# Optimization experiments

Measured on AMD Instinct MI355X. Metric: run time of the kernel, lower is better.

Reference implementation:

```python
import jax, jax.numpy as jnp
import numpy as np
import math

B, NQ, D = 2, 5000, 256
HEADS, LVLS, PTS, NREF = 8, 4, 8, 4  # PTS = all_sampling_points, NREF = ref points per query
DH = D // HEADS
SHAPES = [(100, 100), (50, 50), (25, 25), (13, 13)]
NV = sum(h * w for h, w in SHAPES)


def _grid_init_bias():
    # replicates DeformableSatAttention.init_weights sampling_offsets bias
    thetas = np.arange(HEADS, dtype=np.float32) * (2.0 * math.pi / HEADS)
    grid = np.stack([np.cos(thetas), np.sin(thetas)], -1)
    grid = grid / np.abs(grid).max(-1, keepdims=True)
    grid = np.tile(grid.reshape(HEADS, 1, 1, 2), (1, LVLS, PTS, 1))  # PTS == HEADS
    for i in range(PTS):
        grid[:, :, i, :] *= i + 1
    return jnp.asarray(grid.reshape(-1), dtype=jnp.float32)


def setup_inputs() -> dict:
    key = jax.random.key(0)
    ks = jax.random.split(key, 8)
    xb = math.sqrt(6.0 / (D + D))  # xavier uniform bound for value_proj
    return {
        "query": jax.random.normal(ks[0], (B, NQ, D), jnp.float32),
        "key": jax.random.normal(ks[1], (B, NV, D), jnp.float32),
        "value": jax.random.normal(ks[2], (B, NV, D), jnp.float32),
        "reference_points": jax.random.uniform(ks[3], (B, NQ, NREF, 2), jnp.float32),
        "spatial_shapes": jnp.asarray(SHAPES, jnp.int32),
        "level_start_index": jnp.asarray(np.cumsum([0] + [h * w for h, w in SHAPES])[:-1], jnp.int32),
        "W_value": jax.random.uniform(ks[4], (D, D), jnp.float32, -xb, xb),
        "b_value": jnp.zeros((D,), jnp.float32),
        "W_offset": 0.01 * jax.random.normal(ks[5], (D, HEADS * LVLS * PTS * 2), jnp.float32),
        "b_offset": _grid_init_bias(),
        "W_attn": 0.01 * jax.random.normal(ks[6], (D, HEADS * LVLS * PTS), jnp.float32),
        "b_attn": jnp.zeros((HEADS * LVLS * PTS,), jnp.float32),
    }


def _bilinear(vflat, H, W, loc):
    # vflat: [B, H*W, HEADS, DH]; loc: [B, NQ, HEADS, PTS, 2] in [0,1]
    # grid_sample-style align_corners=False, zero padding (as in MSDeformAttn CUDA)
    x = loc[..., 0] * W - 0.5
    y = loc[..., 1] * H - 0.5
    x0 = jnp.floor(x)
    y0 = jnp.floor(y)
    dx = x - x0
    dy = y - y0
    x0i = x0.astype(jnp.int32)
    y0i = y0.astype(jnp.int32)

    def gather(ix, iy):
        valid = ((ix >= 0) & (ix < W) & (iy >= 0) & (iy < H)).astype(vflat.dtype)
        idx = jnp.clip(iy, 0, H - 1) * W + jnp.clip(ix, 0, W - 1)  # [B,NQ,HEADS,PTS]
        b, nq, h, p = idx.shape
        idx2 = idx.transpose(0, 1, 3, 2).reshape(b, nq * p, h)
        g = jnp.take_along_axis(vflat, idx2[..., None], axis=1)  # [B,NQ*PTS,HEADS,DH]
        g = g.reshape(b, nq, p, h, -1).transpose(0, 1, 3, 2, 4)  # [B,NQ,HEADS,PTS,DH]
        return g * valid[..., None]

    g00 = gather(x0i, y0i)
    g01 = gather(x0i + 1, y0i)
    g10 = gather(x0i, y0i + 1)
    g11 = gather(x0i + 1, y0i + 1)
    w00 = ((1 - dx) * (1 - dy))[..., None]
    w01 = (dx * (1 - dy))[..., None]
    w10 = ((1 - dx) * dy)[..., None]
    w11 = (dx * dy)[..., None]
    return g00 * w00 + g01 * w01 + g10 * w10 + g11 * w11


def reference(query, key, value, reference_points, spatial_shapes, level_start_index,
              W_value, b_value, W_offset, b_offset, W_attn, b_attn):
    bs, nq, _ = query.shape
    v = (value @ W_value + b_value).reshape(bs, -1, HEADS, DH)
    off = (query @ W_offset + b_offset).reshape(bs, nq, HEADS, LVLS, PTS, 2)
    aw = jax.nn.softmax((query @ W_attn + b_attn).reshape(bs, nq, HEADS, LVLS * PTS), axis=-1)
    aw = aw.reshape(bs, nq, HEADS, LVLS, PTS)
    shapes = np.asarray(spatial_shapes)  # static level geometry
    starts = np.asarray(level_start_index)
    # offset_normalizer = (W, H) per level
    norm = jnp.asarray(np.stack([shapes[:, 1], shapes[:, 0]], -1), jnp.float32)
    off = off / norm[None, None, None, :, None, :]
    off = off.reshape(bs, nq, HEADS, LVLS, PTS // NREF, NREF, 2)
    loc = reference_points[:, :, None, None, None, :, :] + off
    loc = loc.reshape(bs, nq, HEADS, LVLS, PTS, 2)
    out = jnp.zeros((bs, nq, HEADS, DH), v.dtype)
    for l in range(shapes.shape[0]):
        Hl, Wl = int(shapes[l, 0]), int(shapes[l, 1])
        s = int(starts[l])
        vl = v[:, s:s + Hl * Wl]
        sampled = _bilinear(vl, Hl, Wl, loc[:, :, :, l])  # [B,NQ,HEADS,PTS,DH]
        out = out + (sampled * aw[:, :, :, l][..., None]).sum(axis=3)
    return out.reshape(bs, nq, D)
```

## Files before the change

### kernel.cpp

```cpp
#include <hip/hip_runtime.h>
#include <math.h>

#define HEADS 8
#define LVLS  4
#define PTS   8
#define NREF  4
#define DH    32
#define DD    256
#define NQc   5000
#define BATCH 2
#define NVc   13294
#define RVr   (BATCH * NVc)
#define RQr   (BATCH * NQc)

#define NJV 832
#define NJQ 942
#define NJOBS (NJV + NJQ)

using f16x8 = __attribute__((ext_vector_type(8))) _Float16;
using f16x4 = __attribute__((ext_vector_type(4))) _Float16;
using f32x4 = __attribute__((ext_vector_type(4))) float;
using h2    = __attribute__((ext_vector_type(2))) _Float16;

__device__ __forceinline__ int pack2(float w) {
    _Float16 h = (_Float16)w;
    h2 v = { h, h };
    return __builtin_bit_cast(int, v);
}

__global__ __launch_bounds__(256) void transpose_w_kernel(
    const float* __restrict__ Wv, const float* __restrict__ Wo,
    const float* __restrict__ Wa,
    _Float16* __restrict__ wtv, _Float16* __restrict__ wto,
    _Float16* __restrict__ wta)
{
    __shared__ float tl[64][65];
    const int bid = blockIdx.x;
    const float* src; _Float16* dst; int N, kt, nt;
    if (bid < 16)      { src = Wv; dst = wtv; N = 256; kt = bid & 3;        nt = bid >> 2; }
    else if (bid < 48) { src = Wo; dst = wto; N = 512; kt = (bid - 16) & 3; nt = (bid - 16) >> 2; }
    else               { src = Wa; dst = wta; N = 256; kt = (bid - 48) & 3; nt = (bid - 48) >> 2; }
    const int k0 = kt * 64, n0 = nt * 64;
    const int c  = threadIdx.x & 63, r4 = threadIdx.x >> 6;
    #pragma unroll
    for (int i = 0; i < 16; ++i) {
        const int r = r4 + i * 4;
        tl[r][c] = src[(size_t)(k0 + r) * N + n0 + c];
    }
    __syncthreads();
    #pragma unroll
    for (int i = 0; i < 16; ++i) {
        const int r = r4 + i * 4;
        dst[(size_t)(n0 + r) * 256 + k0 + c] = (_Float16)tl[c][r];
    }
}

__global__ __launch_bounds__(256) void gemm_uber_kernel(
    const float* __restrict__ value, const float* __restrict__ query,
    const _Float16* __restrict__ wtv, const _Float16* __restrict__ wtoa,
    const float* __restrict__ bv, const float* __restrict__ bo,
    const float* __restrict__ ba,
    _Float16* __restrict__ v_f16, _Float16* __restrict__ offa)
{
    __shared__ _Float16 aL[64][72];
    __shared__ _Float16 bL[128][64];

    const int t    = threadIdx.x;
    const int lane = t & 63;
    const int wid  = t >> 6;
    const int wr   = wid >> 1;
    const int wc   = wid & 1;

    const int job = blockIdx.x;
    const bool isV = job < NJV;
    const float* A; const _Float16* WT; int R, r0, ct;
    if (isV) { A = value; WT = wtv;  R = RVr; r0 = (job >> 1) * 64;  ct = job & 1; }
    else     { const int j2 = job - NJV;
               A = query; WT = wtoa; R = RQr; r0 = (j2 / 6) * 64;    ct = j2 % 6; }
    const int c0 = ct * 128;

    f32x4 acc[2][4] = {};

    const int sr = t >> 4;
    const int sc = (t & 15) * 4;
    const int brow  = lane >> 3;
    const int bslot = (lane & 7) ^ brow;

    for (int kc = 0; kc < 256; kc += 64) {
        __syncthreads();
        #pragma unroll
        for (int cch = 0; cch < 4; ++cch) {
            const int ch  = wid * 4 + cch;
            const int row = ch * 8 + brow;
            const _Float16* src = WT + (size_t)(c0 + row) * 256 + kc + bslot * 8;
            char* ldst = (char*)&bL[0][0] + ch * 1024;
            __builtin_amdgcn_global_load_lds(
                (const __attribute__((address_space(1))) void*)src,
                (__attribute__((address_space(3))) void*)ldst, 16, 0, 0);
        }
        #pragma unroll
        for (int i = 0; i < 4; ++i) {
            const int row = sr + i * 16;
            const int gr  = r0 + row;
            float4 vv = make_float4(0.f, 0.f, 0.f, 0.f);
            if (gr < R) vv = *(const float4*)&A[(size_t)gr * 256 + kc + sc];
            f16x4 pk = { (_Float16)vv.x, (_Float16)vv.y, (_Float16)vv.z, (_Float16)vv.w };
            *(f16x4*)&aL[row][sc] = pk;
        }
        __syncthreads();

        const int lm  = lane & 15;
        const int khi = lane >> 4;
        const char* bB = (const char*)&bL[0][0];
        #pragma unroll
        for (int kk = 0; kk < 2; ++kk) {
            f16x8 bfrag[4];
            #pragma unroll
            for (int nf = 0; nf < 4; ++nf) {
                const int row  = wc * 64 + nf * 16 + lm;
                const int slot = kk * 4 + khi;
                bfrag[nf] = *(const f16x8*)(bB + row * 128 + ((slot ^ (row & 7)) << 4));
            }
            #pragma unroll
            for (int m = 0; m < 2; ++m) {
                const f16x8 afrag = *(const f16x8*)&aL[wr * 32 + m * 16 + lm][kk * 32 + khi * 8];
                #pragma unroll
                for (int nf = 0; nf < 4; ++nf)
                    acc[m][nf] = __builtin_amdgcn_mfma_f32_16x16x32_f16(
                        afrag, bfrag[nf], acc[m][nf], 0, 0, 0);
            }
        }
    }

    const int lm = lane & 15;
    const int lq = lane >> 4;
    if (isV) {
        #pragma unroll
        for (int nf = 0; nf < 4; ++nf) {
            const int col = c0 + wc * 64 + nf * 16 + lm;
            const int hh = col >> 5, ch = col & 31;
            const float bb = bv[col];
            #pragma unroll
            for (int m = 0; m < 2; ++m)
                #pragma unroll
                for (int r = 0; r < 4; ++r) {
                    const int row = r0 + wr * 32 + m * 16 + lq * 4 + r;
                    if (row < RVr) {
                        const int b   = (row >= NVc) ? 1 : 0;
                        const int pix = row - b * NVc;
                        v_f16[(((size_t)(b * HEADS + hh) * NVc) + pix) * 32 + ch] =
                            (_Float16)(acc[m][nf][r] + bb);
                    }
                }
        }
    } else {
        #pragma unroll
        for (int nf = 0; nf < 4; ++nf) {
            const int col = c0 + wc * 64 + nf * 16 + lm;
            const float bb = (col < 512) ? bo[col] : ba[col - 512];
            #pragma unroll
            for (int m = 0; m < 2; ++m)
                #pragma unroll
                for (int r = 0; r < 4; ++r) {
                    const int row = r0 + wr * 32 + m * 16 + lq * 4 + r;
                    if (row < RQr) offa[(size_t)row * 768 + col] = (_Float16)(acc[m][nf][r] + bb);
                }
        }
    }
}

__global__ __launch_bounds__(256) void sample_kernel(
    const _Float16* __restrict__ v,
    const _Float16* __restrict__ offa,
    const float* __restrict__ refp,
    float* __restrict__ out)
{
    __shared__ int2 swa[4][32][5];

    const int t    = threadIdx.x;
    const int wv   = t >> 6;
    const int lane = t & 63;
    const int j    = lane & 31;
    const int half = lane >> 5;

    const int task = blockIdx.x * 4 + wv;
    const int h  = task & 7;
    const int bq = task >> 3;
    const int b  = bq / NQc;

    {
        const int l = j >> 3;
        const int p = j & 7;
        const int r = p & 3;
        const int   Wi = (l == 0) ? 100 : (l == 1) ? 50 : (l == 2) ? 25 : 13;
        const float Wf = (float)Wi;
        const int   st = (l == 0) ? 0 : (l == 1) ? 10000 : (l == 2) ? 12500 : 13125;

        const _Float16* orow = offa + (size_t)bq * 768;
        const float lg = (float)orow[512 + h * 32 + j];
        const float e  = __expf(lg);
        float s = e;
        #pragma unroll
        for (int mask = 16; mask >= 1; mask >>= 1)
            s += __shfl_xor(s, mask, 64);
        const float aw = __fdividef(e, s);

        const h2 oxy = *(const h2*)&orow[h * 64 + j * 2];
        const float2 rxy = *(const float2*)&refp[((size_t)bq * NREF + r) * 2];

        const float x = rxy.x * Wf + (float)oxy[0] - 0.5f;
        const float y = rxy.y * Wf + (float)oxy[1] - 0.5f;
        const float x0f = floorf(x), y0f = floorf(y);
        const float dx = x - x0f, dy = y - y0f;
        const int x0 = (int)x0f, y0 = (int)y0f;
        const int x1 = x0 + 1;

        const int   yy = y0 + half;
        const float fy = (half ? dy : 1.f - dy) * aw;
        const bool  vy = (yy >= 0) && (yy < Wi);
        const int   yc = min(max(yy, 0), Wi - 1);

        const bool vx0 = (x0 >= 0) && (x0 < Wi);
        const bool vx1 = (x1 >= 0) && (x1 < Wi);
        const int  xc0 = min(max(x0, 0), Wi - 1);
        const int  xc1 = min(max(x1, 0), Wi - 1);

        const int bb   = ((b * HEADS + h) * NVc + st) * 64;
        const int rowb = bb + yc * Wi * 64;
        const float wA = (vx0 && vy) ? (1.f - dx) * fy : 0.f;
        const float wB = (vx1 && vy) ? dx * fy : 0.f;

        swa[wv][j][half * 2 + 0] = make_int2(rowb + (xc0 << 6), pack2(wA));
        swa[wv][j][half * 2 + 1] = make_int2(rowb + (xc1 << 6), pack2(wB));
    }

    const int po  = lane >> 4;
    const int c   = (lane >> 2) & 3;
    const int cqb = (lane & 3) * 16;

    int2 aw8[8];
    #pragma unroll
    for (int it = 0; it < 8; ++it)
        aw8[it] = swa[wv][it * 4 + po][c];

    f16x8 val[8];
    #pragma unroll
    for (int it = 0; it < 8; ++it)
        val[it] = *(const f16x8*)((const char*)v + aw8[it].x + cqb);

    h2 acc0 = {}, acc1 = {}, acc2 = {}, acc3 = {};
    #pragma unroll
    for (int it = 0; it < 8; ++it) {
        const h2 w2 = __builtin_bit_cast(h2, aw8[it].y);
        acc0 += w2 * (h2){ val[it][0], val[it][1] };
        acc1 += w2 * (h2){ val[it][2], val[it][3] };
        acc2 += w2 * (h2){ val[it][4], val[it][5] };
        acc3 += w2 * (h2){ val[it][6], val[it][7] };
    }

    #pragma unroll
    for (int mask = 4; mask <= 32; mask <<= 1) {
        acc0 += __builtin_bit_cast(h2, __shfl_xor(__builtin_bit_cast(int, acc0), mask, 64));
        acc1 += __builtin_bit_cast(h2, __shfl_xor(__builtin_bit_cast(int, acc1), mask, 64));
        acc2 += __builtin_bit_cast(h2, __shfl_xor(__builtin_bit_cast(int, acc2), mask, 64));
        acc3 += __builtin_bit_cast(h2, __shfl_xor(__builtin_bit_cast(int, acc3), mask, 64));
    }

    if (lane < 4) {
        float* dst = &out[(size_t)bq * 256 + h * 32 + lane * 8];
        *(float4*)(dst + 0) = make_float4((float)acc0[0], (float)acc0[1],
                                          (float)acc1[0], (float)acc1[1]);
        *(float4*)(dst + 4) = make_float4((float)acc2[0], (float)acc2[1],
                                          (float)acc3[0], (float)acc3[1]);
    }
}

extern "C" void kernel_launch(void* const* d_in, const int* in_sizes, int n_in,
                              void* d_out, int out_size, void* d_ws, size_t ws_size,
                              hipStream_t stream)
{
    const float* query  = (const float*)d_in[0];
    const float* value  = (const float*)d_in[2];
    const float* refp   = (const float*)d_in[3];
    const float* Wv     = (const float*)d_in[6];
    const float* bv     = (const float*)d_in[7];
    const float* Wo     = (const float*)d_in[8];
    const float* bo     = (const float*)d_in[9];
    const float* Wa     = (const float*)d_in[10];
    const float* ba     = (const float*)d_in[11];
    float* out = (float*)d_out;

    _Float16* v_f16 = (_Float16*)d_ws;
    _Float16* offa  = v_f16 + (size_t)RVr * 256;
    _Float16* wtv   = offa + (size_t)RQr * 768;
    _Float16* wtoa  = wtv + 256 * 256;

    transpose_w_kernel<<<dim3(64), 256, 0, stream>>>(
        Wv, Wo, Wa, wtv, wtoa, wtoa + 512 * 256);

    gemm_uber_kernel<<<dim3(NJOBS), 256, 0, stream>>>(
        value, query, wtv, wtoa, bv, bo, ba, v_f16, offa);

    sample_kernel<<<dim3(RQr * HEADS / 4), 256, 0, stream>>>(
        v_f16, offa, refp, out);
}
```

Before: 80.64 us.

## Pre-convert activations to fp16 and stream GEMM A tiles via async LDS loads

The weight-transpose kernel becomes a prep kernel that also converts the value and query activations from fp32 to fp16 into workspace buffers. The GEMM then fetches its A tiles with global_load_lds direct-to-LDS loads into an XOR-swizzled layout, the same scheme already used for B, instead of loading fp32, converting in registers and storing to LDS. The aim is to cut register and VALU work in the GEMM main loop and to halve the bytes it reads for repeatedly loaded A tiles. The cost is an extra full fp32 read plus fp16 write pass over the activations. The per-row bounds checks are also dropped, so tail tiles read padding rows from neighbouring workspace memory; their stores remain guarded.

```diff
diff --git a/kernel.cpp b/kernel.cpp
--- a/kernel.cpp
+++ b/kernel.cpp
@@ -17,6 +17,11 @@
 #define NJQ 942
 #define NJOBS (NJV + NJQ)
 
+#define NEV (RVr * 256)
+#define NEQ (RQr * 256)
+#define NCV ((NEV + 4095) / 4096)
+#define NCQ ((NEQ + 4095) / 4096)
+
 using f16x8 = __attribute__((ext_vector_type(8))) _Float16;
 using f16x4 = __attribute__((ext_vector_type(4))) _Float16;
 using f32x4 = __attribute__((ext_vector_type(4))) float;
@@ -28,41 +33,60 @@
     return __builtin_bit_cast(int, v);
 }
 
-__global__ __launch_bounds__(256) void transpose_w_kernel(
+__global__ __launch_bounds__(256) void prep_kernel(
+    const float* __restrict__ value, const float* __restrict__ query,
     const float* __restrict__ Wv, const float* __restrict__ Wo,
     const float* __restrict__ Wa,
+    _Float16* __restrict__ a16v, _Float16* __restrict__ a16q,
     _Float16* __restrict__ wtv, _Float16* __restrict__ wto,
     _Float16* __restrict__ wta)
 {
-    __shared__ float tl[64][65];
     const int bid = blockIdx.x;
-    const float* src; _Float16* dst; int N, kt, nt;
-    if (bid < 16)      { src = Wv; dst = wtv; N = 256; kt = bid & 3;        nt = bid >> 2; }
-    else if (bid < 48) { src = Wo; dst = wto; N = 512; kt = (bid - 16) & 3; nt = (bid - 16) >> 2; }
-    else               { src = Wa; dst = wta; N = 256; kt = (bid - 48) & 3; nt = (bid - 48) >> 2; }
-    const int k0 = kt * 64, n0 = nt * 64;
-    const int c  = threadIdx.x & 63, r4 = threadIdx.x >> 6;
-    #pragma unroll
-    for (int i = 0; i < 16; ++i) {
-        const int r = r4 + i * 4;
-        tl[r][c] = src[(size_t)(k0 + r) * N + n0 + c];
-    }
-    __syncthreads();
-    #pragma unroll
-    for (int i = 0; i < 16; ++i) {
-        const int r = r4 + i * 4;
-        dst[(size_t)(n0 + r) * 256 + k0 + c] = (_Float16)tl[c][r];
+    const int t   = threadIdx.x;
+    if (bid < 64) {
+        __shared__ float tl[64][65];
+        const float* src; _Float16* dst; int N, kt, nt;
+        if (bid < 16)      { src = Wv; dst = wtv; N = 256; kt = bid & 3;        nt = bid >> 2; }
+        else if (bid < 48) { src = Wo; dst = wto; N = 512; kt = (bid - 16) & 3; nt = (bid - 16) >> 2; }
+        else               { src = Wa; dst = wta; N = 256; kt = (bid - 48) & 3; nt = (bid - 48) >> 2; }
+        const int k0 = kt * 64, n0 = nt * 64;
+        const int c  = t & 63, r4 = t >> 6;
+        #pragma unroll
+        for (int i = 0; i < 16; ++i) {
+            const int r = r4 + i * 4;
+            tl[r][c] = src[(size_t)(k0 + r) * N + n0 + c];
+        }
+        __syncthreads();
+        #pragma unroll
+        for (int i = 0; i < 16; ++i) {
+            const int r = r4 + i * 4;
+            dst[(size_t)(n0 + r) * 256 + k0 + c] = (_Float16)tl[c][r];
+        }
+        return;
+    }
+    const int cid = bid - 64;
+    const float* src; _Float16* dst; int n; size_t base;
+    if (cid < NCV) { src = value; dst = a16v; n = NEV; base = (size_t)cid * 4096; }
+    else           { src = query; dst = a16q; n = NEQ; base = (size_t)(cid - NCV) * 4096; }
+    #pragma unroll
+    for (int i = 0; i < 4; ++i) {
+        const size_t idx = base + i * 1024 + t * 4;
+        if (idx < (size_t)n) {
+            const float4 v = *(const float4*)&src[idx];
+            f16x4 pk = { (_Float16)v.x, (_Float16)v.y, (_Float16)v.z, (_Float16)v.w };
+            *(f16x4*)&dst[idx] = pk;
+        }
     }
 }
 
 __global__ __launch_bounds__(256) void gemm_uber_kernel(
-    const float* __restrict__ value, const float* __restrict__ query,
+    const _Float16* __restrict__ a16v, const _Float16* __restrict__ a16q,
     const _Float16* __restrict__ wtv, const _Float16* __restrict__ wtoa,
     const float* __restrict__ bv, const float* __restrict__ bo,
     const float* __restrict__ ba,
     _Float16* __restrict__ v_f16, _Float16* __restrict__ offa)
 {
-    __shared__ _Float16 aL[64][72];
+    __shared__ _Float16 aL[64][64];
     __shared__ _Float16 bL[128][64];
 
     const int t    = threadIdx.x;
@@ -73,18 +97,18 @@
 
     const int job = blockIdx.x;
     const bool isV = job < NJV;
-    const float* A; const _Float16* WT; int R, r0, ct;
-    if (isV) { A = value; WT = wtv;  R = RVr; r0 = (job >> 1) * 64;  ct = job & 1; }
+    const _Float16* A; const _Float16* WT; int r0, ct;
+    if (isV) { A = a16v; WT = wtv;  r0 = (job >> 1) * 64;  ct = job & 1; }
     else     { const int j2 = job - NJV;
-               A = query; WT = wtoa; R = RQr; r0 = (j2 / 6) * 64;    ct = j2 % 6; }
+               A = a16q; WT = wtoa; r0 = (j2 / 6) * 64;    ct = j2 % 6; }
     const int c0 = ct * 128;
 
     f32x4 acc[2][4] = {};
 
-    const int sr = t >> 4;
-    const int sc = (t & 15) * 4;
     const int brow  = lane >> 3;
     const int bslot = (lane & 7) ^ brow;
+    const int lm  = lane & 15;
+    const int khi = lane >> 4;
 
     for (int kc = 0; kc < 256; kc += 64) {
         __syncthreads();
@@ -99,31 +123,32 @@
                 (__attribute__((address_space(3))) void*)ldst, 16, 0, 0);
         }
         #pragma unroll
-        for (int i = 0; i < 4; ++i) {
-            const int row = sr + i * 16;
-            const int gr  = r0 + row;
-            float4 vv = make_float4(0.f, 0.f, 0.f, 0.f);
-            if (gr < R) vv = *(const float4*)&A[(size_t)gr * 256 + kc + sc];
-            f16x4 pk = { (_Float16)vv.x, (_Float16)vv.y, (_Float16)vv.z, (_Float16)vv.w };
-            *(f16x4*)&aL[row][sc] = pk;
+        for (int cch = 0; cch < 2; ++cch) {
+            const int ch  = wid * 2 + cch;
+            const int row = ch * 8 + brow;
+            const _Float16* src = A + (size_t)(r0 + row) * 256 + kc + bslot * 8;
+            char* ldst = (char*)&aL[0][0] + ch * 1024;
+            __builtin_amdgcn_global_load_lds(
+                (const __attribute__((address_space(1))) void*)src,
+                (__attribute__((address_space(3))) void*)ldst, 16, 0, 0);
         }
         __syncthreads();
 
-        const int lm  = lane & 15;
-        const int khi = lane >> 4;
         const char* bB = (const char*)&bL[0][0];
+        const char* aB = (const char*)&aL[0][0];
         #pragma unroll
         for (int kk = 0; kk < 2; ++kk) {
+            const int slot = kk * 4 + khi;
             f16x8 bfrag[4];
             #pragma unroll
             for (int nf = 0; nf < 4; ++nf) {
-                const int row  = wc * 64 + nf * 16 + lm;
-                const int slot = kk * 4 + khi;
+                const int row = wc * 64 + nf * 16 + lm;
                 bfrag[nf] = *(const f16x8*)(bB + row * 128 + ((slot ^ (row & 7)) << 4));
             }
             #pragma unroll
             for (int m = 0; m < 2; ++m) {
-                const f16x8 afrag = *(const f16x8*)&aL[wr * 32 + m * 16 + lm][kk * 32 + khi * 8];
+                const int arow = wr * 32 + m * 16 + lm;
+                const f16x8 afrag = *(const f16x8*)(aB + arow * 128 + ((slot ^ (arow & 7)) << 4));
                 #pragma unroll
                 for (int nf = 0; nf < 4; ++nf)
                     acc[m][nf] = __builtin_amdgcn_mfma_f32_16x16x32_f16(
@@ -132,7 +157,6 @@
         }
     }
 
-    const int lm = lane & 15;
     const int lq = lane >> 4;
     if (isV) {
         #pragma unroll
@@ -290,16 +314,18 @@
     const float* ba     = (const float*)d_in[11];
     float* out = (float*)d_out;
 
-    _Float16* v_f16 = (_Float16*)d_ws;
+    _Float16* a16v  = (_Float16*)d_ws;
+    _Float16* a16q  = a16v + (size_t)RVr * 256;
+    _Float16* v_f16 = a16q + (size_t)RQr * 256;
     _Float16* offa  = v_f16 + (size_t)RVr * 256;
     _Float16* wtv   = offa + (size_t)RQr * 768;
     _Float16* wtoa  = wtv + 256 * 256;
 
-    transpose_w_kernel<<<dim3(64), 256, 0, stream>>>(
-        Wv, Wo, Wa, wtv, wtoa, wtoa + 512 * 256);
+    prep_kernel<<<dim3(64 + NCV + NCQ), 256, 0, stream>>>(
+        value, query, Wv, Wo, Wa, a16v, a16q, wtv, wtoa, wtoa + 512 * 256);
 
     gemm_uber_kernel<<<dim3(NJOBS), 256, 0, stream>>>(
-        value, query, wtv, wtoa, bv, bo, ba, v_f16, offa);
+        a16v, a16q, wtv, wtoa, bv, bo, ba, v_f16, offa);
 
     sample_kernel<<<dim3(RQr * HEADS / 4), 256, 0, stream>>>(
         v_f16, offa, refp, out);
```

Measured after the change: 76.56 us. -5.1%, faster.
